# Kernel optimization log

Measured on AMD Instinct MI355X. Metric: run time of the kernel, lower is better.

Reference implementation:

```python
import jax, jax.numpy as jnp
import numpy as np

B, E, O, H = 4096, 1024, 16, 1024  # batch, embed_dim, num_ops, hidden_dim


def setup_inputs() -> dict:
    key = jax.random.key(0)
    k1, k2, k3, k4, k5, k6 = jax.random.split(key, 6)
    s1 = 1.0 / np.sqrt(E)
    s2 = 1.0 / np.sqrt(H)
    return {
        "x_aug": jax.random.normal(k1, (B, E), dtype=jnp.float32),
        "op_idx": jax.random.randint(k2, (B,), 0, O, dtype=jnp.int32),
        "W1": jax.random.normal(k3, (E, O, H), dtype=jnp.float32) * s1,  # DenseGeneral kernel: embed -> (ops, hidden)
        "b1": jnp.zeros((O, H), dtype=jnp.float32),
        "W2": jax.random.normal(k4, (H, O, H), dtype=jnp.float32) * s2,  # per-op second layer (diagonal of DenseGeneral)
        "b2": jnp.zeros((O, H), dtype=jnp.float32),
    }


def reference(x_aug, op_idx, W1, b1, W2, b2):
    # h1[b,o,h] = relu(sum_e x[b,e] W1[e,o,h] + b1[o,h])
    h1 = jax.nn.relu(jnp.einsum("be,eoh->boh", x_aug, W1) + b1)
    # h2[b,o,g] = relu(sum_h h1[b,o,h] W2[h,o,g] + b2[o,g])  (per-op MLP)
    h2 = jax.nn.relu(jnp.einsum("boh,hog->bog", h1, W2) + b2)
    # select the chosen operator's output per example
    idx = jnp.broadcast_to(op_idx[:, None, None], (x_aug.shape[0], 1, h2.shape[-1]))
    return jnp.take_along_axis(h2, idx, axis=1).squeeze(1)  # [B, H]
```

## Files before the change

kernel.cpp:

```cpp
#include <hip/hip_runtime.h>

#define Bn 4096
#define En 1024
#define On 16
#define Hn 1024
#define OHn (On * Hn)

#define BM 64
#define BN 128
#define BK 64
#define MAXT 80

using floatx4 = __attribute__((ext_vector_type(4))) float;
using float4v = __attribute__((ext_vector_type(4))) float;
using bf16x8  = __attribute__((ext_vector_type(8))) __bf16;
using short8v = __attribute__((ext_vector_type(8))) short;
using short4v = __attribute__((ext_vector_type(4))) short;

__device__ inline unsigned short f2bf(float f) {
    unsigned u = __builtin_bit_cast(unsigned, f);
    u += 0x7fffu + ((u >> 16) & 1u);
    return (unsigned short)(u >> 16);
}

__device__ __forceinline__ void gld16(const unsigned short* g, unsigned short* l) {
    __builtin_amdgcn_global_load_lds(
        (const __attribute__((address_space(1))) unsigned int*)g,
        (__attribute__((address_space(3))) unsigned int*)l, 16, 0, 0);
}

__global__ void bucket_kernel(const int* __restrict__ op_idx,
                              int* __restrict__ sorted_idx,
                              int* __restrict__ offsets,
                              int* __restrict__ tile_o,
                              int* __restrict__ tile_m) {
    __shared__ int cnt[On], cur[On], off[On + 1];
    int tid = threadIdx.x;
    if (tid < On) { cnt[tid] = 0; cur[tid] = 0; }
    __syncthreads();
    for (int i = tid; i < Bn; i += blockDim.x) atomicAdd(&cnt[op_idx[i]], 1);
    __syncthreads();
    if (tid == 0) {
        int s = 0;
        for (int o = 0; o < On; ++o) { off[o] = s; s += cnt[o]; }
        off[On] = s;
        int nt = 0;
        for (int o = 0; o < On; ++o)
            for (int m0 = 0; m0 < cnt[o]; m0 += BM) { tile_o[nt] = o; tile_m[nt] = m0; ++nt; }
        for (; nt < MAXT; ++nt) { tile_o[nt] = -1; tile_m[nt] = 0; }
    }
    __syncthreads();
    for (int i = tid; i < Bn; i += blockDim.x) {
        int o = op_idx[i];
        int p = off[o] + atomicAdd(&cur[o], 1);
        sorted_idx[p] = i;
    }
    if (tid <= On) offsets[tid] = off[tid];
}

__device__ __forceinline__ void pack_w_block4(const float* __restrict__ W,
                                              unsigned short* __restrict__ Wp,
                                              int o, int g, int t) {
    int h0 = t * 4;
    const float* src = W + (size_t)(g * 8) * OHn + (size_t)o * Hn + h0;
    float4v v[8];
#pragma unroll
    for (int j = 0; j < 8; ++j) v[j] = *(const float4v*)(src + (size_t)j * OHn);
    unsigned short* dst = Wp + (((size_t)o * 128 + g) * Hn + h0) * 8;
#pragma unroll
    for (int hh = 0; hh < 4; ++hh) {
        short8v w;
#pragma unroll
        for (int j = 0; j < 8; ++j) w[j] = (short)f2bf(v[j][hh]);
        *(short8v*)(dst + hh * 8) = w;
    }
}

__global__ __launch_bounds__(256) void pack1_kernel(
    const float* __restrict__ W1, const float* __restrict__ x,
    const int* __restrict__ sorted_idx,
    unsigned short* __restrict__ Wp1, unsigned short* __restrict__ x_s) {
    int b = blockIdx.x, t = threadIdx.x;
    if (b < 2048) {
        pack_w_block4(W1, Wp1, b >> 7, b & 127, t);
    } else {
        int p0 = (b - 2048) * 4;
#pragma unroll
        for (int r = 0; r < 4; ++r) {
            int p = p0 + r;
            int row = sorted_idx[p];
            float4v v = *(const float4v*)(x + (size_t)row * En + t * 4);
            short4v w;
#pragma unroll
            for (int j = 0; j < 4; ++j) w[j] = (short)f2bf(v[j]);
            *(short4v*)&x_s[(size_t)p * En + t * 4] = w;
        }
    }
}

__global__ __launch_bounds__(256) void pack_w_kernel(const float* __restrict__ W,
                                                     unsigned short* __restrict__ Wp) {
    int b = blockIdx.x;
    pack_w_block4(W, Wp, b >> 7, b & 127, threadIdx.x);
}

__global__ __launch_bounds__(256) void gemm1_kernel(
    const unsigned short* __restrict__ x_s, const unsigned short* __restrict__ Wp,
    const float* __restrict__ bias1, const int* __restrict__ offsets,
    const int* __restrict__ tile_o, const int* __restrict__ tile_m,
    unsigned short* __restrict__ h1,
    const float* __restrict__ W2, unsigned short* __restrict__ Wp2) {
    int yy = blockIdx.y;
    int tid = threadIdx.x;
    if (yy >= MAXT) {
        if (W2 != nullptr && Wp2 != nullptr) {
            int p = (yy - MAXT) * 8 + blockIdx.x;
            pack_w_block4(W2, Wp2, p >> 7, p & 127, tid);
        }
        return;
    }
    int o = tile_o[yy];
    if (o < 0) return;
    int m0 = tile_m[yy];
    int off = offsets[o];
    int cnt = offsets[o + 1] - off;
    int n0 = blockIdx.x * BN;

    __shared__ __attribute__((aligned(16))) unsigned short As[2][8][BM][8];
    __shared__ __attribute__((aligned(16))) unsigned short Bs[2][8][BN][8];

    int arow = tid & 63, ag = tid >> 6;
    int rr = m0 + arow; if (rr >= cnt) rr = cnt - 1;
    const unsigned short* aBase = x_s + (size_t)(off + rr) * En;

    int bn = tid & 127, bg = tid >> 7;
    const unsigned short* bBase = Wp + (((size_t)o * 128 + bg) * Hn + n0 + bn) * 8;

    auto STAGE = [&](int buf, int kt) {
        gld16(aBase + kt + ag * 8,        &As[buf][ag][arow][0]);
        gld16(aBase + kt + (ag + 4) * 8,  &As[buf][ag + 4][arow][0]);
        const unsigned short* bk = bBase + (size_t)kt * Hn;
#pragma unroll
        for (int i = 0; i < 4; ++i)
            gld16(bk + (size_t)i * (2 * Hn * 8), &Bs[buf][bg + 2 * i][bn][0]);
    };

    floatx4 acc[2][4] = {};
    int lane = tid & 63, wave = tid >> 6;
    int wm = (wave >> 1) * 32, wn = (wave & 1) * 64;
    int l15 = lane & 15, kg = lane >> 4;

    auto COMPUTE = [&](int buf) {
#pragma unroll
        for (int ks = 0; ks < 2; ++ks) {
            int g = ks * 4 + kg;
            bf16x8 af[2], bfr[4];
#pragma unroll
            for (int mt = 0; mt < 2; ++mt) af[mt] = *(const bf16x8*)&As[buf][g][wm + mt * 16 + l15][0];
#pragma unroll
            for (int nt = 0; nt < 4; ++nt) bfr[nt] = *(const bf16x8*)&Bs[buf][g][wn + nt * 16 + l15][0];
#pragma unroll
            for (int mt = 0; mt < 2; ++mt)
#pragma unroll
                for (int nt = 0; nt < 4; ++nt)
                    acc[mt][nt] = __builtin_amdgcn_mfma_f32_16x16x32_bf16(af[mt], bfr[nt], acc[mt][nt], 0, 0, 0);
        }
    };

    STAGE(0, 0);
    for (int kt = 0; kt < En; kt += 2 * BK) {
        __syncthreads();
        STAGE(1, kt + BK);
        COMPUTE(0);
        __syncthreads();
        if (kt + 2 * BK < En) STAGE(0, kt + 2 * BK);
        COMPUTE(1);
    }

    int r4 = (lane >> 4) * 4;
#pragma unroll
    for (int nt = 0; nt < 4; ++nt) {
        int col = n0 + wn + nt * 16 + l15;
        float bv = bias1[o * Hn + col];
#pragma unroll
        for (int mt = 0; mt < 2; ++mt) {
#pragma unroll
            for (int r = 0; r < 4; ++r) {
                int row = m0 + wm + mt * 16 + r4 + r;
                if (row < cnt) {
                    float v = acc[mt][nt][r] + bv;
                    v = v > 0.f ? v : 0.f;
                    h1[(size_t)(off + row) * Hn + col] = f2bf(v);
                }
            }
        }
    }
}

__global__ __launch_bounds__(256) void gemm2_kernel(
    const unsigned short* __restrict__ h1, const unsigned short* __restrict__ Wp,
    const float* __restrict__ bias2, const int* __restrict__ sorted_idx,
    const int* __restrict__ offsets, const int* __restrict__ tile_o,
    const int* __restrict__ tile_m, float* __restrict__ out) {
    int o = tile_o[blockIdx.y];
    if (o < 0) return;
    int m0 = tile_m[blockIdx.y];
    int off = offsets[o];
    int cnt = offsets[o + 1] - off;
    int n0 = blockIdx.x * BN;

    __shared__ __attribute__((aligned(16))) unsigned short As[2][8][BM][8];
    __shared__ __attribute__((aligned(16))) unsigned short Bs[2][8][BN][8];

    int tid = threadIdx.x;

    int arow = tid & 63, ag = tid >> 6;
    int rr = m0 + arow; if (rr >= cnt) rr = cnt - 1;
    const unsigned short* aBase = h1 + (size_t)(off + rr) * Hn;

    int bn = tid & 127, bg = tid >> 7;
    const unsigned short* bBase = Wp + (((size_t)o * 128 + bg) * Hn + n0 + bn) * 8;

    auto STAGE = [&](int buf, int kt) {
        gld16(aBase + kt + ag * 8,        &As[buf][ag][arow][0]);
        gld16(aBase + kt + (ag + 4) * 8,  &As[buf][ag + 4][arow][0]);
        const unsigned short* bk = bBase + (size_t)kt * Hn;
#pragma unroll
        for (int i = 0; i < 4; ++i)
            gld16(bk + (size_t)i * (2 * Hn * 8), &Bs[buf][bg + 2 * i][bn][0]);
    };

    floatx4 acc[2][4] = {};
    int lane = tid & 63, wave = tid >> 6;
    int wm = (wave >> 1) * 32, wn = (wave & 1) * 64;
    int l15 = lane & 15, kg = lane >> 4;

    auto COMPUTE = [&](int buf) {
#pragma unroll
        for (int ks = 0; ks < 2; ++ks) {
            int g = ks * 4 + kg;
            bf16x8 af[2], bfr[4];
#pragma unroll
            for (int mt = 0; mt < 2; ++mt) af[mt] = *(const bf16x8*)&As[buf][g][wm + mt * 16 + l15][0];
#pragma unroll
            for (int nt = 0; nt < 4; ++nt) bfr[nt] = *(const bf16x8*)&Bs[buf][g][wn + nt * 16 + l15][0];
#pragma unroll
            for (int mt = 0; mt < 2; ++mt)
#pragma unroll
                for (int nt = 0; nt < 4; ++nt)
                    acc[mt][nt] = __builtin_amdgcn_mfma_f32_16x16x32_bf16(af[mt], bfr[nt], acc[mt][nt], 0, 0, 0);
        }
    };

    STAGE(0, 0);
    for (int kt = 0; kt < Hn; kt += 2 * BK) {
        __syncthreads();
        STAGE(1, kt + BK);
        COMPUTE(0);
        __syncthreads();
        if (kt + 2 * BK < Hn) STAGE(0, kt + 2 * BK);
        COMPUTE(1);
    }

    int r4 = (lane >> 4) * 4;
    float bv[4];
#pragma unroll
    for (int nt = 0; nt < 4; ++nt) bv[nt] = bias2[o * Hn + n0 + wn + nt * 16 + l15];
#pragma unroll
    for (int mt = 0; mt < 2; ++mt) {
#pragma unroll
        for (int r = 0; r < 4; ++r) {
            int row = m0 + wm + mt * 16 + r4 + r;
            if (row < cnt) {
                int b = sorted_idx[off + row];
                float* orow = out + (size_t)b * Hn + n0 + wn + l15;
#pragma unroll
                for (int nt = 0; nt < 4; ++nt) {
                    float v = acc[mt][nt][r] + bv[nt];
                    orow[nt * 16] = v > 0.f ? v : 0.f;
                }
            }
        }
    }
}

extern "C" void kernel_launch(void* const* d_in, const int* in_sizes, int n_in,
                              void* d_out, int out_size, void* d_ws, size_t ws_size,
                              hipStream_t stream) {
    const float* x      = (const float*)d_in[0];
    const int*   op_idx = (const int*)d_in[1];
    const float* W1     = (const float*)d_in[2];
    const float* bias1  = (const float*)d_in[3];
    const float* W2     = (const float*)d_in[4];
    const float* bias2  = (const float*)d_in[5];
    float* out = (float*)d_out;

    char* ws = (char*)d_ws;
    int* offsets    = (int*)ws;
    int* sorted_idx = (int*)(ws + 256);
    int* tile_o     = (int*)(ws + 16640);
    int* tile_m     = (int*)(ws + 17152);

    const size_t HDR       = 32768;
    const size_t X_S_ELEMS = (size_t)Bn * En;
    const size_t H1_ELEMS  = (size_t)Bn * Hn;
    const size_t WP_ELEMS  = (size_t)On * 128 * Hn * 8;
    const size_t need_full = HDR + 2 * (X_S_ELEMS + H1_ELEMS + 2 * WP_ELEMS);
    const size_t need_half = HDR + 2 * (X_S_ELEMS + H1_ELEMS + WP_ELEMS);

    unsigned short* x_s = (unsigned short*)(ws + HDR);
    unsigned short* h1  = x_s + X_S_ELEMS;
    unsigned short* Wp1 = h1 + H1_ELEMS;
    unsigned short* Wp2 = Wp1 + WP_ELEMS;

    hipLaunchKernelGGL(bucket_kernel, dim3(1), dim3(1024), 0, stream,
                       op_idx, sorted_idx, offsets, tile_o, tile_m);

    if (ws_size >= need_full) {
        hipLaunchKernelGGL(pack1_kernel, dim3(3072), dim3(256), 0, stream,
                           W1, x, sorted_idx, Wp1, x_s);
        hipLaunchKernelGGL(gemm1_kernel, dim3(Hn / BN, MAXT + 256), dim3(256), 0, stream,
                           x_s, Wp1, bias1, offsets, tile_o, tile_m, h1, W2, Wp2);
        hipLaunchKernelGGL(gemm2_kernel, dim3(Hn / BN, MAXT), dim3(256), 0, stream,
                           h1, Wp2, bias2, sorted_idx, offsets, tile_o, tile_m, out);
    } else if (ws_size >= need_half) {
        hipLaunchKernelGGL(pack1_kernel, dim3(3072), dim3(256), 0, stream,
                           W1, x, sorted_idx, Wp1, x_s);
        hipLaunchKernelGGL(gemm1_kernel, dim3(Hn / BN, MAXT), dim3(256), 0, stream,
                           x_s, Wp1, bias1, offsets, tile_o, tile_m, h1,
                           (const float*)nullptr, (unsigned short*)nullptr);
        hipLaunchKernelGGL(pack_w_kernel, dim3(2048), dim3(256), 0, stream,
                           W2, Wp1);
        hipLaunchKernelGGL(gemm2_kernel, dim3(Hn / BN, MAXT), dim3(256), 0, stream,
                           h1, Wp1, bias2, sorted_idx, offsets, tile_o, tile_m, out);
    }
}
```

Measured before the change: 247.5 us.

## Overlap next-tile global loads with MFMA using explicit vmcnt waits and barriers

Reworks the double-buffered K loop in both GEMM kernels so the load for the next stage is issued before waiting. The wait is a partial s_waitcnt vmcnt(6) plus a raw s_barrier instead of __syncthreads, which drains all outstanding loads. The loop is fully unrolled with sched_barrier fences to keep the compiler from reordering across stages. The aim is to keep one tile's global->LDS loads in flight during compute. It relies on the vmcnt value matching exactly the number of loads per STAGE, which is fragile if STAGE's load count differs.

```diff
diff --git a/kernel.cpp b/kernel.cpp
--- a/kernel.cpp
+++ b/kernel.cpp
@@ -28,6 +28,11 @@
         (const __attribute__((address_space(1))) unsigned int*)g,
         (__attribute__((address_space(3))) unsigned int*)l, 16, 0, 0);
 }
+
+#define VMCNT6() asm volatile("s_waitcnt vmcnt(6)" ::: "memory")
+#define VMCNT0() asm volatile("s_waitcnt vmcnt(0)" ::: "memory")
+#define SBAR()   __builtin_amdgcn_s_barrier()
+#define SCHED0() __builtin_amdgcn_sched_barrier(0)
 
 __global__ void bucket_kernel(const int* __restrict__ op_idx,
                               int* __restrict__ sorted_idx,
@@ -168,14 +173,23 @@
     };
 
     STAGE(0, 0);
-    for (int kt = 0; kt < En; kt += 2 * BK) {
-        __syncthreads();
-        STAGE(1, kt + BK);
+    STAGE(1, BK);
+#pragma unroll
+    for (int ii = 0; ii < 7; ++ii) {
+        VMCNT6(); SBAR(); SCHED0();
         COMPUTE(0);
-        __syncthreads();
-        if (kt + 2 * BK < En) STAGE(0, kt + 2 * BK);
+        SCHED0(); SBAR(); SCHED0();
+        STAGE(0, (2 * ii + 2) * BK);
+        VMCNT6(); SBAR(); SCHED0();
         COMPUTE(1);
-    }
+        SCHED0(); SBAR(); SCHED0();
+        STAGE(1, (2 * ii + 3) * BK);
+    }
+    VMCNT6(); SBAR(); SCHED0();
+    COMPUTE(0);
+    SCHED0(); SBAR(); SCHED0();
+    VMCNT0(); SBAR(); SCHED0();
+    COMPUTE(1);
 
     int r4 = (lane >> 4) * 4;
 #pragma unroll
@@ -253,14 +267,23 @@
     };
 
     STAGE(0, 0);
-    for (int kt = 0; kt < Hn; kt += 2 * BK) {
-        __syncthreads();
-        STAGE(1, kt + BK);
+    STAGE(1, BK);
+#pragma unroll
+    for (int ii = 0; ii < 7; ++ii) {
+        VMCNT6(); SBAR(); SCHED0();
         COMPUTE(0);
-        __syncthreads();
-        if (kt + 2 * BK < Hn) STAGE(0, kt + 2 * BK);
+        SCHED0(); SBAR(); SCHED0();
+        STAGE(0, (2 * ii + 2) * BK);
+        VMCNT6(); SBAR(); SCHED0();
         COMPUTE(1);
-    }
+        SCHED0(); SBAR(); SCHED0();
+        STAGE(1, (2 * ii + 3) * BK);
+    }
+    VMCNT6(); SBAR(); SCHED0();
+    COMPUTE(0);
+    SCHED0(); SBAR(); SCHED0();
+    VMCNT0(); SBAR(); SCHED0();
+    COMPUTE(1);
 
     int r4 = (lane >> 4) * 4;
     float bv[4];
```

Result: no change. 250.3 us (+1.1%).
